# Optimization experiments

Measured on AMD Instinct MI355X. Metric: run time of the kernel, lower is better.

The kernel has to match this reference:

```python
import jax, jax.numpy as jnp
import numpy as np
import math

B, S, D = 4, 1024, 1024
H, DK = 16, 64
NUM_BUCKETS = 32
MAX_DISTANCE = 128


def _relative_position_bucket(relative_position, bidirectional=True,
                              num_buckets=32, max_distance=128):
    # faithful port of T5's bucketing
    relative_buckets = jnp.zeros_like(relative_position)
    if bidirectional:
        num_buckets //= 2
        relative_buckets = relative_buckets + (relative_position > 0).astype(jnp.int32) * num_buckets
        relative_position = jnp.abs(relative_position)
    else:
        relative_position = -jnp.minimum(relative_position, jnp.zeros_like(relative_position))
    max_exact = num_buckets // 2
    is_small = relative_position < max_exact
    rp_safe = jnp.maximum(relative_position, 1)  # avoid log(0); masked by is_small
    rel_if_large = max_exact + (
        jnp.log(rp_safe.astype(jnp.float32) / max_exact)
        / math.log(max_distance / max_exact) * (num_buckets - max_exact)
    ).astype(jnp.int32)
    rel_if_large = jnp.minimum(rel_if_large, num_buckets - 1)
    return relative_buckets + jnp.where(is_small, relative_position, rel_if_large)


def compute_bias(rel_bias_emb, query_length, key_length):
    ctx = jnp.arange(query_length, dtype=jnp.int32)[:, None]
    mem = jnp.arange(key_length, dtype=jnp.int32)[None, :]
    rp = mem - ctx  # [q, k]
    buckets = _relative_position_bucket(rp, bidirectional=True,
                                        num_buckets=NUM_BUCKETS,
                                        max_distance=MAX_DISTANCE)
    values = rel_bias_emb[buckets]          # [q, k, h]
    return jnp.transpose(values, (2, 0, 1))[None]  # [1, h, q, k]


def setup_inputs() -> dict:
    key = jax.random.key(0)
    ks = jax.random.split(key, 6)
    s = 1.0 / math.sqrt(D)
    return {
        "hidden_states": jax.random.normal(ks[0], (B, S, D), jnp.float32),
        "Wq": jax.random.normal(ks[1], (D, H * DK), jnp.float32) * s,
        "Wk": jax.random.normal(ks[2], (D, H * DK), jnp.float32) * s,
        "Wv": jax.random.normal(ks[3], (D, H * DK), jnp.float32) * s,
        "Wo": jax.random.normal(ks[4], (H * DK, D), jnp.float32) * s,
        "rel_bias_emb": jax.random.normal(ks[5], (NUM_BUCKETS, H), jnp.float32),
    }


def reference(hidden_states, Wq, Wk, Wv, Wo, rel_bias_emb):
    b, s, _ = hidden_states.shape

    def shape_heads(x):  # [b, s, h*dk] -> [b, h, s, dk]
        return x.reshape(b, s, H, DK).transpose(0, 2, 1, 3)

    q = shape_heads(hidden_states @ Wq)
    k = shape_heads(hidden_states @ Wk)
    v = shape_heads(hidden_states @ Wv)

    # T5 attention: no 1/sqrt(dk) scaling
    scores = jnp.einsum('bhqd,bhkd->bhqk', q, k)
    position_bias = compute_bias(rel_bias_emb, s, s)  # [1, h, s, s]
    scores = scores + position_bias
    attn = jax.nn.softmax(scores.astype(jnp.float32), axis=-1).astype(scores.dtype)
    ctx = jnp.einsum('bhqk,bhkd->bhqd', attn, v)
    ctx = ctx.transpose(0, 2, 1, 3).reshape(b, s, H * DK)
    return ctx @ Wo
```

## Files before the change

kernel.cpp:

```cpp
#include <hip/hip_runtime.h>

typedef unsigned short u16;
typedef unsigned int u32;
typedef __bf16 bf16x8 __attribute__((ext_vector_type(8)));
typedef float f32x4 __attribute__((ext_vector_type(4)));

#define MFMA16(a, b, c) __builtin_amdgcn_mfma_f32_16x16x32_bf16(a, b, c, 0, 0, 0)
#define LOG2E 1.4426950408889634f

__device__ __forceinline__ u16 f2bf(float f) {
  u32 u = __float_as_uint(f);
  u += 0x7FFFu + ((u >> 16) & 1u);
  return (u16)(u >> 16);
}

__device__ __forceinline__ void gld16(u16* lds, const u16* g) {
  __builtin_amdgcn_global_load_lds((const __attribute__((address_space(1))) void*)g,
                                   (__attribute__((address_space(3))) void*)lds,
                                   16, 0, 0);
}

__device__ __forceinline__ int t5_bucket(int rp) {
  int ret = rp > 0 ? 16 : 0;
  int a = rp < 0 ? -rp : rp;
  int b;
  if      (a <  8) b = a;
  else if (a < 12) b = 8;
  else if (a < 16) b = 9;
  else if (a < 23) b = 10;
  else if (a < 32) b = 11;
  else if (a < 46) b = 12;
  else if (a < 64) b = 13;
  else if (a < 91) b = 14;
  else             b = 15;
  return ret + b;
}

__global__ __launch_bounds__(256) void prep(const float4* __restrict__ X, ushort4* __restrict__ Xb,
                                            const float* __restrict__ w0, const float* __restrict__ w1,
                                            const float* __restrict__ w2, const float* __restrict__ w3,
                                            u16* __restrict__ out) {
  int bid = blockIdx.x;
  if (bid < 512) {
#pragma unroll
    for (int i = 0; i < 8; i++) {
      int g = bid * 2048 + i * 256 + threadIdx.x;
      float4 v = X[g];
      ushort4 o;
      o.x = f2bf(v.x); o.y = f2bf(v.y); o.z = f2bf(v.z); o.w = f2bf(v.w);
      Xb[g] = o;
    }
    return;
  }
  bid -= 512;
  __shared__ __align__(16) u16 tb[64 * 68];
  const int col = threadIdx.x & 63;
  const int rowo = threadIdx.x >> 6;
#pragma unroll 1
  for (int t2 = 0; t2 < 2; t2++) {
    const int tile = bid * 2 + t2;
    const int z = tile >> 8, t = tile & 255;
    const float* W = (z == 0) ? w0 : (z == 1) ? w1 : (z == 2) ? w2 : w3;
    u16* O = out + z * 1048576;
    const int n0 = (t & 15) * 64, k0 = (t >> 4) * 64;
#pragma unroll
    for (int r = 0; r < 16; r++) {
      int kl = r * 4 + rowo;
      tb[col * 68 + kl] = f2bf(W[(k0 + kl) * 1024 + n0 + col]);
    }
    __syncthreads();
#pragma unroll
    for (int r = 0; r < 16; r++) {
      int nl = r * 4 + rowo;
      O[(n0 + nl) * 1024 + k0 + col] = tb[nl * 68 + col];
    }
    __syncthreads();
  }
}

__global__ __launch_bounds__(256) void gemm128(const u16* __restrict__ A,
                                               const u16* __restrict__ BtBase,
                                               u16* __restrict__ outp) {
  __shared__ __align__(16) u16 smem[18432];
  const int tid = threadIdx.x, lane = tid & 63, wave = tid >> 6;
  const int l15 = lane & 15, quad = lane >> 4;
  const int wm = (wave >> 1) * 64, wn = (wave & 1) * 64;

  const int id = blockIdx.x + blockIdx.y * 24;
  const int xcd = id & 7, jj = id >> 3;
  const int nz = (jj % 12) + (xcd & 1) * 12;
  const int ymb = (jj / 12) + (xcd >> 1) * 8;
  const int n = nz / 3, z = nz % 3;
  const int m0 = ymb * 128, n0 = n * 128;
  const u16* Ab = A + m0 * 1024;
  const u16* Bb = BtBase + z * 1048576 + n0 * 1024;

  int cc0 = tid, cc1 = 256 + tid;
  int row0 = cc0 >> 2, row1 = cc1 >> 2;
  int aoff0 = row0 * 1024 + (((cc0 & 3) ^ ((row0 >> 1) & 3)) * 8);
  int aoff1 = row1 * 1024 + (((cc1 & 3) ^ ((row1 >> 1) & 3)) * 8);

  f32x4 acc[4][4];
  const f32x4 vz = {0.f, 0.f, 0.f, 0.f};
#pragma unroll
  for (int i = 0; i < 4; i++)
#pragma unroll
    for (int j = 0; j < 4; j++) acc[i][j] = vz;

  const int sk = (l15 >> 1) & 3;

  {
    u16* st = smem;
    gld16(st + cc0 * 8, Ab + aoff0);
    gld16(st + cc1 * 8, Ab + aoff1);
    gld16(st + 4096 + cc0 * 8, Bb + aoff0);
    gld16(st + 4096 + cc1 * 8, Bb + aoff1);
  }

#pragma unroll 1
  for (int kt = 0; kt < 32; kt++) {
    u16* st = smem + (kt & 1) * 8192;
    if (kt < 31) {
      u16* dst = smem + ((kt + 1) & 1) * 8192;
      const int ka = (kt + 1) * 32;
      gld16(dst + cc0 * 8, Ab + ka + aoff0);
      gld16(dst + cc1 * 8, Ab + ka + aoff1);
      gld16(dst + 4096 + cc0 * 8, Bb + ka + aoff0);
      gld16(dst + 4096 + cc1 * 8, Bb + ka + aoff1);
      asm volatile("s_waitcnt vmcnt(4)\n\ts_barrier" ::: "memory");
    } else {
      asm volatile("s_waitcnt vmcnt(0)\n\ts_barrier" ::: "memory");
    }
    bf16x8 af[4], bg[4];
#pragma unroll
    for (int mt = 0; mt < 4; mt++)
      af[mt] = *(const bf16x8*)(st + (wm + mt * 16 + l15) * 32 + ((quad ^ sk) * 8));
#pragma unroll
    for (int nt = 0; nt < 4; nt++)
      bg[nt] = *(const bf16x8*)(st + 4096 + (wn + nt * 16 + l15) * 32 + ((quad ^ sk) * 8));
#pragma unroll
    for (int mt = 0; mt < 4; mt++)
#pragma unroll
      for (int nt = 0; nt < 4; nt++)
        acc[mt][nt] = MFMA16(af[mt], bg[nt], acc[mt][nt]);
    asm volatile("s_barrier" ::: "memory");
  }
  __syncthreads();

  if (z == 2) {
    u16* O = outp + z * 4194304;
#pragma unroll
    for (int mt = 0; mt < 4; mt++)
#pragma unroll
      for (int nt = 0; nt < 4; nt++) {
        int col = wn + nt * 16 + l15;
        int rowb = wm + mt * 16 + quad * 4;
        uint2 p;
        p.x = (u32)f2bf(acc[mt][nt][0]) | ((u32)f2bf(acc[mt][nt][1]) << 16);
        p.y = (u32)f2bf(acc[mt][nt][2]) | ((u32)f2bf(acc[mt][nt][3]) << 16);
        *(uint2*)(smem + col * 136 + rowb) = p;
      }
    __syncthreads();
    const int b = m0 >> 10, sbase = m0 & 1023;
#pragma unroll
    for (int p = 0; p < 8; p++) {
      int g = p * 256 + tid;
      int col = g >> 4, chunk = g & 15;
      uint4 v = *(const uint4*)(smem + col * 136 + chunk * 8);
      int nn = n0 + col, hh = nn >> 6, dk = nn & 63;
      *(uint4*)(O + ((b * 16 + hh) * 64 + dk) * 1024 + sbase + chunk * 8) = v;
    }
  } else {
    u16* O = outp + z * 4194304;
    const float scl = (z == 0) ? LOG2E : 1.0f;
#pragma unroll
    for (int mt = 0; mt < 4; mt++)
#pragma unroll
      for (int nt = 0; nt < 4; nt++) {
        int rowb = wm + mt * 16 + quad * 4;
        int colb = wn + nt * 16 + l15;
#pragma unroll
        for (int reg = 0; reg < 4; reg++)
          smem[(rowb + reg) * 144 + colb] = f2bf(acc[mt][nt][reg] * scl);
      }
    __syncthreads();
    const int b = m0 >> 10, sbase = m0 & 1023;
#pragma unroll
    for (int p = 0; p < 8; p++) {
      int g = p * 256 + tid;
      int ml = g >> 4, c = g & 15;
      uint4 v = *(const uint4*)(smem + ml * 144 + c * 8);
      int nn = n0 + c * 8, hh = nn >> 6, dk = nn & 63;
      *(uint4*)(O + (b * 16 + hh) * 65536 + (sbase + ml) * 64 + dk) = v;
    }
  }
}

__global__ __launch_bounds__(256) void attn(const u16* __restrict__ Q, const u16* __restrict__ K,
                                            const u16* __restrict__ V, const float* __restrict__ emb,
                                            u16* __restrict__ ctx) {
  __shared__ __align__(16) u16 sK[64 * 64];
  __shared__ __align__(16) u16 sV[64 * 64];
  __shared__ __align__(16) u16 sP[128 * 72];
  __shared__ __align__(16) float4 bt4[1156];
  const int tid = threadIdx.x, lane = tid & 63, wave = tid >> 6;
  const int l15 = lane & 15, quad = lane >> 4;
  const int bh = blockIdx.x, qt = blockIdx.y;
  const int h = bh & 15, b = bh >> 4;
  const u16* Qp = Q + bh * 65536 + qt * 8192;
  const u16* Kp = K + bh * 65536;
  const u16* Vp = V + bh * 65536;
  const int sx = l15 & 7;

  bf16x8 aq[2][2];
#pragma unroll
  for (int u = 0; u < 2; u++)
#pragma unroll
    for (int kk = 0; kk < 2; kk++)
      aq[u][kk] = *(const bf16x8*)(Qp + (wave * 32 + u * 16 + l15) * 64 + kk * 32 + quad * 8);

  for (int i = tid; i < 1156; i += 256) {
    int rp0 = i - 127 - qt * 128;
    float4 v;
    v.x = emb[t5_bucket(rp0)     * 16 + h] * LOG2E;
    v.y = emb[t5_bucket(rp0 + 1) * 16 + h] * LOG2E;
    v.z = emb[t5_bucket(rp0 + 2) * 16 + h] * LOG2E;
    v.w = emb[t5_bucket(rp0 + 3) * 16 + h] * LOG2E;
    bt4[i] = v;
  }
  const float bias_pos = emb[31 * 16 + h] * LOG2E;
  const float bias_neg = emb[15 * 16 + h] * LOG2E;

  float2 ls2[2] = {{0.f, 0.f}, {0.f, 0.f}};
  f32x4 oc[2][4];
  const f32x4 vzero = {0.f, 0.f, 0.f, 0.f};
#pragma unroll
  for (int u = 0; u < 2; u++)
#pragma unroll
    for (int nt = 0; nt < 4; nt++) oc[u][nt] = vzero;

  __syncthreads();

#pragma unroll 1
  for (int j = 0; j < 16; j++) {
    const u16* Kj = Kp + j * 4096;
#pragma unroll
    for (int r = 0; r < 2; r++) {
      int cb = r * 256 + wave * 64;
      int cc = cb + lane;
      int row = cc >> 3, c8 = (cc & 7) ^ (row & 7);
      gld16(sK + cb * 8, Kj + row * 64 + c8 * 8);
      gld16(sV + cb * 8, Vp + row * 1024 + j * 64 + c8 * 8);
    }
    __syncthreads();

    f32x4 sc[4][2];
    const int rp_min = j * 64 - qt * 128 - 127;
    const int rp_max = j * 64 + 63 - qt * 128;
    if (rp_min >= 91) {
#pragma unroll
      for (int mt = 0; mt < 4; mt++)
#pragma unroll
        for (int u = 0; u < 2; u++) { sc[mt][u][0] = bias_pos; sc[mt][u][1] = bias_pos; sc[mt][u][2] = bias_pos; sc[mt][u][3] = bias_pos; }
    } else if (rp_max <= -91) {
#pragma unroll
      for (int mt = 0; mt < 4; mt++)
#pragma unroll
        for (int u = 0; u < 2; u++) { sc[mt][u][0] = bias_neg; sc[mt][u][1] = bias_neg; sc[mt][u][2] = bias_neg; sc[mt][u][3] = bias_neg; }
    } else {
#pragma unroll
      for (int mt = 0; mt < 4; mt++)
#pragma unroll
        for (int u = 0; u < 2; u++) {
          int idx = j * 64 + mt * 16 + quad * 4 - wave * 32 - u * 16 - l15 + 127;
          float4 bv4 = bt4[idx];
          sc[mt][u][0] = bv4.x; sc[mt][u][1] = bv4.y; sc[mt][u][2] = bv4.z; sc[mt][u][3] = bv4.w;
        }
    }
#pragma unroll
    for (int kk = 0; kk < 2; kk++) {
      bf16x8 ak[4];
      int g8 = kk * 4 + quad;
#pragma unroll
      for (int mt = 0; mt < 4; mt++)
        ak[mt] = *(const bf16x8*)(sK + (mt * 16 + l15) * 64 + (g8 ^ sx) * 8);
#pragma unroll
      for (int mt = 0; mt < 4; mt++)
#pragma unroll
        for (int u = 0; u < 2; u++)
          sc[mt][u] = MFMA16(ak[mt], aq[u][kk], sc[mt][u]);
    }

#pragma unroll
    for (int u = 0; u < 2; u++) {
      const int prow = wave * 32 + u * 16 + l15;
#pragma unroll
      for (int mt = 0; mt < 4; mt++) {
        u32 b0 = __float_as_uint(__builtin_amdgcn_exp2f(sc[mt][u][0]));
        u32 b1 = __float_as_uint(__builtin_amdgcn_exp2f(sc[mt][u][1]));
        u32 b2 = __float_as_uint(__builtin_amdgcn_exp2f(sc[mt][u][2]));
        u32 b3 = __float_as_uint(__builtin_amdgcn_exp2f(sc[mt][u][3]));
        u32 t0 = b0 & 0xFFFF0000u, t1 = b1 & 0xFFFF0000u;
        u32 t2 = b2 & 0xFFFF0000u, t3 = b3 & 0xFFFF0000u;
        ls2[u].x += __uint_as_float(t0) + __uint_as_float(t2);
        ls2[u].y += __uint_as_float(t1) + __uint_as_float(t3);
        uint2 pk;
        pk.x = (t0 >> 16) | t1;
        pk.y = (t2 >> 16) | t3;
        *(uint2*)(sP + prow * 72 + mt * 16 + quad * 4) = pk;
      }
    }
    asm volatile("s_waitcnt lgkmcnt(0)" ::: "memory");

#pragma unroll
    for (int kk = 0; kk < 2; kk++) {
      bf16x8 ap[2];
      int g8 = kk * 4 + quad;
#pragma unroll
      for (int u = 0; u < 2; u++)
        ap[u] = *(const bf16x8*)(sP + (wave * 32 + u * 16 + l15) * 72 + kk * 32 + quad * 8);
#pragma unroll
      for (int nt = 0; nt < 4; nt++) {
        bf16x8 bv = *(const bf16x8*)(sV + (nt * 16 + l15) * 64 + (g8 ^ sx) * 8);
#pragma unroll
        for (int u = 0; u < 2; u++)
          oc[u][nt] = MFMA16(ap[u], bv, oc[u][nt]);
      }
    }
    __syncthreads();
  }

  float lsum[2];
#pragma unroll
  for (int u = 0; u < 2; u++) {
    lsum[u] = ls2[u].x + ls2[u].y;
    lsum[u] += __shfl_xor(lsum[u], 16, 64);
    lsum[u] += __shfl_xor(lsum[u], 32, 64);
  }
  float linv[2][4];
#pragma unroll
  for (int u = 0; u < 2; u++)
#pragma unroll
    for (int reg = 0; reg < 4; reg++)
      linv[u][reg] = __builtin_amdgcn_rcpf(__shfl(lsum[u], quad * 4 + reg, 64));

  u16* cb2 = ctx + b * 1048576 + (qt * 128 + wave * 32) * 1024 + h * 64;
#pragma unroll
  for (int u = 0; u < 2; u++)
#pragma unroll
    for (int nt = 0; nt < 4; nt++)
#pragma unroll
      for (int reg = 0; reg < 4; reg++)
        cb2[(u * 16 + quad * 4 + reg) * 1024 + nt * 16 + l15] = f2bf(oc[u][nt][reg] * linv[u][reg]);
}

__global__ __launch_bounds__(256) void gemm_o(const u16* __restrict__ A,
                                              const u16* __restrict__ Bt,
                                              float* __restrict__ O) {
  __shared__ __align__(16) u16 smem[24576];
  const int tid = threadIdx.x, lane = tid & 63, wave = tid >> 6;
  const int l15 = lane & 15, quad = lane >> 4;
  const int m0 = blockIdx.x * 64, n0 = blockIdx.y * 128;
  const u16* Ab = A + m0 * 1024;
  const u16* Bb = Bt + n0 * 1024;
  const int wn = wave * 32;

  int ac = tid, bc0 = tid, bc1 = 256 + tid, bc2 = 512 + tid, bc3 = 768 + tid;
  int ar0 = tid >> 3, ar1 = (256 + tid) >> 3;
  int aoff0 = ar0 * 1024 + (((tid & 7) ^ (ar0 & 7)) * 8);
  int aoff1 = ar1 * 1024 + ((((256 + tid) & 7) ^ (ar1 & 7)) * 8);
  int boff[4], bdst[4];
#pragma unroll
  for (int r = 0; r < 4; r++) {
    int cc = r * 256 + tid;
    int row = cc >> 3;
    boff[r] = row * 1024 + (((cc & 7) ^ (row & 7)) * 8);
    bdst[r] = cc * 8;
  }

  f32x4 acc[4][2];
  const f32x4 vz = {0.f, 0.f, 0.f, 0.f};
#pragma unroll
  for (int i = 0; i < 4; i++) { acc[i][0] = vz; acc[i][1] = vz; }

  const int sx = l15 & 7;

  {
    u16* st = smem;
    gld16(st + tid * 8, Ab + aoff0);
    gld16(st + (256 + tid) * 8, Ab + aoff1);
#pragma unroll
    for (int r = 0; r < 4; r++) gld16(st + 4096 + bdst[r], Bb + boff[r]);
  }

#pragma unroll 1
  for (int kt = 0; kt < 16; kt++) {
    u16* st = smem + (kt & 1) * 12288;
    if (kt < 15) {
      u16* dst = smem + ((kt + 1) & 1) * 12288;
      const int ka = (kt + 1) * 64;
      gld16(dst + tid * 8, Ab + ka + aoff0);
      gld16(dst + (256 + tid) * 8, Ab + ka + aoff1);
#pragma unroll
      for (int r = 0; r < 4; r++) gld16(dst + 4096 + bdst[r], Bb + ka + boff[r]);
      asm volatile("s_waitcnt vmcnt(6)\n\ts_barrier" ::: "memory");
    } else {
      asm volatile("s_waitcnt vmcnt(0)\n\ts_barrier" ::: "memory");
    }
#pragma unroll
    for (int kk = 0; kk < 2; kk++) {
      bf16x8 af[4], bg[2];
      int g8 = kk * 4 + quad;
#pragma unroll
      for (int mt = 0; mt < 4; mt++)
        af[mt] = *(const bf16x8*)(st + (mt * 16 + l15) * 64 + ((g8 ^ sx) * 8));
#pragma unroll
      for (int nt = 0; nt < 2; nt++)
        bg[nt] = *(const bf16x8*)(st + 4096 + (wn + nt * 16 + l15) * 64 + ((g8 ^ sx) * 8));
#pragma unroll
      for (int mt = 0; mt < 4; mt++)
#pragma unroll
        for (int nt = 0; nt < 2; nt++)
          acc[mt][nt] = MFMA16(af[mt], bg[nt], acc[mt][nt]);
    }
    asm volatile("s_barrier" ::: "memory");
  }

#pragma unroll
  for (int mt = 0; mt < 4; mt++)
#pragma unroll
    for (int nt = 0; nt < 2; nt++)
#pragma unroll
      for (int reg = 0; reg < 4; reg++) {
        int row = m0 + mt * 16 + quad * 4 + reg;
        int col = n0 + wn + nt * 16 + l15;
        O[row * 1024 + col] = acc[mt][nt][reg];
      }
}

extern "C" void kernel_launch(void* const* d_in, const int* in_sizes, int n_in,
                              void* d_out, int out_size, void* d_ws, size_t ws_size,
                              hipStream_t stream) {
  (void)in_sizes; (void)n_in; (void)out_size; (void)ws_size;
  const float* X   = (const float*)d_in[0];
  const float* Wq  = (const float*)d_in[1];
  const float* Wk  = (const float*)d_in[2];
  const float* Wv  = (const float*)d_in[3];
  const float* Wo  = (const float*)d_in[4];
  const float* emb = (const float*)d_in[5];

  char* ws = (char*)d_ws;
  u16* Xb  = (u16*)(ws);
  u16* Wt  = (u16*)(ws + (8u  << 20));
  u16* Qb  = (u16*)(ws + (16u << 20));
  u16* Ctx = (u16*)(ws + (40u << 20));

  prep<<<1024, 256, 0, stream>>>((const float4*)X, (ushort4*)Xb, Wq, Wk, Wv, Wo, Wt);
  gemm128<<<dim3(24, 32), 256, 0, stream>>>(Xb, Wt, Qb);
  attn<<<dim3(64, 8), 256, 0, stream>>>(Qb, Qb + 4194304, Qb + 2 * 4194304, emb, Ctx);
  gemm_o<<<dim3(64, 8), 256, 0, stream>>>(Ctx, Wt + 3 * 1048576, (float*)d_out);
}
```

Before: 164.8 us.

## Triple-buffer GEMM loads and double-buffer K/V tiles in attention

Both GEMM kernels go from a two-stage to a three-stage LDS ring, prefetching two k-tiles ahead and waiting with deeper vmcnt thresholds to hide more global-load latency. The attention kernel now double-buffers its K/V tiles, issuing the next block's async loads before computing on the current one, and swaps a __syncthreads for a bare barrier. The cost is more LDS per block (gemm128 to 48KB, gemm_o to 72KB, attn larger), which may cut occupancy.

```diff
diff --git a/kernel.cpp b/kernel.cpp
--- a/kernel.cpp
+++ b/kernel.cpp
@@ -81,7 +81,7 @@
 __global__ __launch_bounds__(256) void gemm128(const u16* __restrict__ A,
                                                const u16* __restrict__ BtBase,
                                                u16* __restrict__ outp) {
-  __shared__ __align__(16) u16 smem[18432];
+  __shared__ __align__(16) u16 smem[24576];
   const int tid = threadIdx.x, lane = tid & 63, wave = tid >> 6;
   const int l15 = lane & 15, quad = lane >> 4;
   const int wm = (wave >> 1) * 64, wn = (wave & 1) * 64;
@@ -110,27 +110,33 @@
   const int sk = (l15 >> 1) & 3;
 
   {
-    u16* st = smem;
-    gld16(st + cc0 * 8, Ab + aoff0);
-    gld16(st + cc1 * 8, Ab + aoff1);
-    gld16(st + 4096 + cc0 * 8, Bb + aoff0);
-    gld16(st + 4096 + cc1 * 8, Bb + aoff1);
-  }
-
+    gld16(smem + cc0 * 8, Ab + aoff0);
+    gld16(smem + cc1 * 8, Ab + aoff1);
+    gld16(smem + 4096 + cc0 * 8, Bb + aoff0);
+    gld16(smem + 4096 + cc1 * 8, Bb + aoff1);
+    gld16(smem + 8192 + cc0 * 8, Ab + 32 + aoff0);
+    gld16(smem + 8192 + cc1 * 8, Ab + 32 + aoff1);
+    gld16(smem + 12288 + cc0 * 8, Bb + 32 + aoff0);
+    gld16(smem + 12288 + cc1 * 8, Bb + 32 + aoff1);
+  }
+
+  int cs = 0, ls = 2;
 #pragma unroll 1
   for (int kt = 0; kt < 32; kt++) {
-    u16* st = smem + (kt & 1) * 8192;
-    if (kt < 31) {
-      u16* dst = smem + ((kt + 1) & 1) * 8192;
-      const int ka = (kt + 1) * 32;
+    if (kt < 30) {
+      u16* dst = smem + ls * 8192;
+      const int ka = (kt + 2) * 32;
       gld16(dst + cc0 * 8, Ab + ka + aoff0);
       gld16(dst + cc1 * 8, Ab + ka + aoff1);
       gld16(dst + 4096 + cc0 * 8, Bb + ka + aoff0);
       gld16(dst + 4096 + cc1 * 8, Bb + ka + aoff1);
+      asm volatile("s_waitcnt vmcnt(8)\n\ts_barrier" ::: "memory");
+    } else if (kt == 30) {
       asm volatile("s_waitcnt vmcnt(4)\n\ts_barrier" ::: "memory");
     } else {
       asm volatile("s_waitcnt vmcnt(0)\n\ts_barrier" ::: "memory");
     }
+    u16* st = smem + cs * 8192;
     bf16x8 af[4], bg[4];
 #pragma unroll
     for (int mt = 0; mt < 4; mt++)
@@ -144,6 +150,8 @@
       for (int nt = 0; nt < 4; nt++)
         acc[mt][nt] = MFMA16(af[mt], bg[nt], acc[mt][nt]);
     asm volatile("s_barrier" ::: "memory");
+    cs = (cs == 2) ? 0 : cs + 1;
+    ls = (ls == 2) ? 0 : ls + 1;
   }
   __syncthreads();
 
@@ -199,8 +207,7 @@
 __global__ __launch_bounds__(256) void attn(const u16* __restrict__ Q, const u16* __restrict__ K,
                                             const u16* __restrict__ V, const float* __restrict__ emb,
                                             u16* __restrict__ ctx) {
-  __shared__ __align__(16) u16 sK[64 * 64];
-  __shared__ __align__(16) u16 sV[64 * 64];
+  __shared__ __align__(16) u16 sKV[2 * 8192];
   __shared__ __align__(16) u16 sP[128 * 72];
   __shared__ __align__(16) float4 bt4[1156];
   const int tid = threadIdx.x, lane = tid & 63, wave = tid >> 6;
@@ -212,12 +219,29 @@
   const u16* Vp = V + bh * 65536;
   const int sx = l15 & 7;
 
+  int koff[2], voff[2], cbs[2];
+#pragma unroll
+  for (int r = 0; r < 2; r++) {
+    int cb = r * 256 + wave * 64;
+    int cc = cb + lane;
+    int row = cc >> 3, c8 = (cc & 7) ^ (row & 7);
+    koff[r] = row * 64 + c8 * 8;
+    voff[r] = row * 1024 + c8 * 8;
+    cbs[r] = cb * 8;
+  }
+
   bf16x8 aq[2][2];
 #pragma unroll
   for (int u = 0; u < 2; u++)
 #pragma unroll
     for (int kk = 0; kk < 2; kk++)
       aq[u][kk] = *(const bf16x8*)(Qp + (wave * 32 + u * 16 + l15) * 64 + kk * 32 + quad * 8);
+
+#pragma unroll
+  for (int r = 0; r < 2; r++) {
+    gld16(sKV + cbs[r], Kp + koff[r]);
+    gld16(sKV + 4096 + cbs[r], Vp + voff[r]);
+  }
 
   for (int i = tid; i < 1156; i += 256) {
     int rp0 = i - 127 - qt * 128;
@@ -243,16 +267,20 @@
 
 #pragma unroll 1
   for (int j = 0; j < 16; j++) {
-    const u16* Kj = Kp + j * 4096;
-#pragma unroll
-    for (int r = 0; r < 2; r++) {
-      int cb = r * 256 + wave * 64;
-      int cc = cb + lane;
-      int row = cc >> 3, c8 = (cc & 7) ^ (row & 7);
-      gld16(sK + cb * 8, Kj + row * 64 + c8 * 8);
-      gld16(sV + cb * 8, Vp + row * 1024 + j * 64 + c8 * 8);
-    }
-    __syncthreads();
+    u16* st = sKV + (j & 1) * 8192;
+    if (j < 15) {
+      u16* dst = sKV + ((j + 1) & 1) * 8192;
+      const u16* Kj1 = Kp + (j + 1) * 4096;
+      const u16* Vj1 = Vp + (j + 1) * 64;
+#pragma unroll
+      for (int r = 0; r < 2; r++) {
+        gld16(dst + cbs[r], Kj1 + koff[r]);
+        gld16(dst + 4096 + cbs[r], Vj1 + voff[r]);
+      }
+      asm volatile("s_waitcnt vmcnt(4)\n\ts_barrier" ::: "memory");
+    } else {
+      asm volatile("s_waitcnt vmcnt(0)\n\ts_barrier" ::: "memory");
+    }
 
     f32x4 sc[4][2];
     const int rp_min = j * 64 - qt * 128 - 127;
@@ -283,7 +311,7 @@
       int g8 = kk * 4 + quad;
 #pragma unroll
       for (int mt = 0; mt < 4; mt++)
-        ak[mt] = *(const bf16x8*)(sK + (mt * 16 + l15) * 64 + (g8 ^ sx) * 8);
+        ak[mt] = *(const bf16x8*)(st + (mt * 16 + l15) * 64 + (g8 ^ sx) * 8);
 #pragma unroll
       for (int mt = 0; mt < 4; mt++)
 #pragma unroll
@@ -321,13 +349,13 @@
         ap[u] = *(const bf16x8*)(sP + (wave * 32 + u * 16 + l15) * 72 + kk * 32 + quad * 8);
 #pragma unroll
       for (int nt = 0; nt < 4; nt++) {
-        bf16x8 bv = *(const bf16x8*)(sV + (nt * 16 + l15) * 64 + (g8 ^ sx) * 8);
+        bf16x8 bv = *(const bf16x8*)(st + 4096 + (nt * 16 + l15) * 64 + (g8 ^ sx) * 8);
 #pragma unroll
         for (int u = 0; u < 2; u++)
           oc[u][nt] = MFMA16(ap[u], bv, oc[u][nt]);
       }
     }
-    __syncthreads();
+    asm volatile("s_barrier" ::: "memory");
   }
 
   float lsum[2];
@@ -357,7 +385,7 @@
 __global__ __launch_bounds__(256) void gemm_o(const u16* __restrict__ A,
                                               const u16* __restrict__ Bt,
                                               float* __restrict__ O) {
-  __shared__ __align__(16) u16 smem[24576];
+  __shared__ __align__(16) u16 smem[36864];
   const int tid = threadIdx.x, lane = tid & 63, wave = tid >> 6;
   const int l15 = lane & 15, quad = lane >> 4;
   const int m0 = blockIdx.x * 64, n0 = blockIdx.y * 128;
@@ -365,7 +393,6 @@
   const u16* Bb = Bt + n0 * 1024;
   const int wn = wave * 32;
 
-  int ac = tid, bc0 = tid, bc1 = 256 + tid, bc2 = 512 + tid, bc3 = 768 + tid;
   int ar0 = tid >> 3, ar1 = (256 + tid) >> 3;
   int aoff0 = ar0 * 1024 + (((tid & 7) ^ (ar0 & 7)) * 8);
   int aoff1 = ar1 * 1024 + ((((256 + tid) & 7) ^ (ar1 & 7)) * 8);
@@ -385,28 +412,33 @@
 
   const int sx = l15 & 7;
 
-  {
-    u16* st = smem;
-    gld16(st + tid * 8, Ab + aoff0);
-    gld16(st + (256 + tid) * 8, Ab + aoff1);
-#pragma unroll
-    for (int r = 0; r < 4; r++) gld16(st + 4096 + bdst[r], Bb + boff[r]);
-  }
-
+#pragma unroll
+  for (int s = 0; s < 2; s++) {
+    u16* st = smem + s * 12288;
+    const int ka = s * 64;
+    gld16(st + tid * 8, Ab + ka + aoff0);
+    gld16(st + (256 + tid) * 8, Ab + ka + aoff1);
+#pragma unroll
+    for (int r = 0; r < 4; r++) gld16(st + 4096 + bdst[r], Bb + ka + boff[r]);
+  }
+
+  int cs = 0, ls = 2;
 #pragma unroll 1
   for (int kt = 0; kt < 16; kt++) {
-    u16* st = smem + (kt & 1) * 12288;
-    if (kt < 15) {
-      u16* dst = smem + ((kt + 1) & 1) * 12288;
-      const int ka = (kt + 1) * 64;
+    if (kt < 14) {
+      u16* dst = smem + ls * 12288;
+      const int ka = (kt + 2) * 64;
       gld16(dst + tid * 8, Ab + ka + aoff0);
       gld16(dst + (256 + tid) * 8, Ab + ka + aoff1);
 #pragma unroll
       for (int r = 0; r < 4; r++) gld16(dst + 4096 + bdst[r], Bb + ka + boff[r]);
+      asm volatile("s_waitcnt vmcnt(12)\n\ts_barrier" ::: "memory");
+    } else if (kt == 14) {
       asm volatile("s_waitcnt vmcnt(6)\n\ts_barrier" ::: "memory");
     } else {
       asm volatile("s_waitcnt vmcnt(0)\n\ts_barrier" ::: "memory");
     }
+    u16* st = smem + cs * 12288;
 #pragma unroll
     for (int kk = 0; kk < 2; kk++) {
       bf16x8 af[4], bg[2];
@@ -424,6 +456,8 @@
           acc[mt][nt] = MFMA16(af[mt], bg[nt], acc[mt][nt]);
     }
     asm volatile("s_barrier" ::: "memory");
+    cs = (cs == 2) ? 0 : cs + 1;
+    ls = (ls == 2) ? 0 : ls + 1;
   }
 
 #pragma unroll
```

After: 163.7 us (median of 2 runs). About the same (-0.7%).
